# Kernel optimization log

Measured on AMD Instinct MI355X. Metric: run time of the kernel, lower is better.

The kernel has to match this reference:

```python
import jax, jax.numpy as jnp
import numpy as np

TAU = 0.05
BIG_POSITIVE = 1.0e10
COS_EPS = 1e-8  # torch F.cosine_similarity default eps


def setup_inputs() -> dict:
    key = jax.random.key(0)
    k1, k2 = jax.random.split(key)
    b, d = 4096, 1024
    return {
        "batch_feat1": jax.random.normal(k1, (b, d), dtype=jnp.float32),
        "batch_feat2": jax.random.normal(k2, (b, d), dtype=jnp.float32),
        "input_mask": jnp.zeros((b,), dtype=jnp.int32),
    }


def reference(batch_feat1, batch_feat2, input_mask):
    # concat the two views: (2b, d)
    feat = jnp.concatenate([batch_feat1, batch_feat2], axis=0)
    bs = feat.shape[0]
    half = bs // 2

    # cosine similarity = normalize (clamped norm, as in torch) then GEMM
    norm = jnp.maximum(jnp.linalg.norm(feat, axis=-1, keepdims=True), COS_EPS)
    n = feat / norm
    similarity = n @ n.T  # (2b, 2b)

    # mask out self-similarity on the diagonal
    eye = jnp.eye(bs, dtype=similarity.dtype)
    logits = similarity / TAU - eye * BIG_POSITIVE

    idx = jnp.arange(half)
    y_true = jnp.concatenate([idx + half, idx])  # positive pair indices

    # weighted cross entropy: weight[c] = 1 - input_mask[c] (per-class weight)
    weight = (1 - jnp.concatenate([input_mask, input_mask], axis=0)).astype(logits.dtype)
    logp = jax.nn.log_softmax(logits, axis=-1)
    per_example = -jnp.take_along_axis(logp, y_true[:, None], axis=1)[:, 0]
    w = weight[y_true]
    loss = jnp.sum(w * per_example) / jnp.sum(w)
    return (loss, logits, y_true)
```

## Files before the change

kernel.cpp:

```cpp
#include <hip/hip_runtime.h>
#include <math.h>

#define BS 8192
#define HALF 4096
#define DIM 1024
#define BIGP 1.0e10f
#define SQRT_TAU_INV 4.472135955f
#define BK 64
#define NT (DIM / BK)

typedef __attribute__((ext_vector_type(8))) short bf16x8;
typedef __attribute__((ext_vector_type(4))) float f32x4;

#define GLOAD_LDS16(g, l)                                              \
    __builtin_amdgcn_global_load_lds(                                  \
        (const __attribute__((address_space(1))) void*)(g),            \
        (__attribute__((address_space(3))) void*)(l), 16, 0, 0)

__device__ inline unsigned short f2bf(float f) {
    union { float f; unsigned int u; } c; c.f = f;
    unsigned int u = c.u;
    u += 0x7FFFu + ((u >> 16) & 1u);
    return (unsigned short)(u >> 16);
}

__global__ __launch_bounds__(256) void norm_kernel(const float* __restrict__ f1,
                                                   const float* __restrict__ f2,
                                                   unsigned short* __restrict__ nb) {
    const int row = blockIdx.x;
    const int t = threadIdx.x;
    const float* src = (row < HALF) ? (f1 + (size_t)row * DIM)
                                    : (f2 + (size_t)(row - HALF) * DIM);
    float4 v = reinterpret_cast<const float4*>(src)[t];
    float ss = v.x * v.x + v.y * v.y + v.z * v.z + v.w * v.w;
#pragma unroll
    for (int off = 32; off > 0; off >>= 1) ss += __shfl_down(ss, off, 64);
    __shared__ float red[4];
    if ((t & 63) == 0) red[t >> 6] = ss;
    __syncthreads();
    float tot = red[0] + red[1] + red[2] + red[3];
    float inv = SQRT_TAU_INV / fmaxf(sqrtf(tot), 1e-8f);
    ushort4 o;
    o.x = f2bf(v.x * inv);
    o.y = f2bf(v.y * inv);
    o.z = f2bf(v.z * inv);
    o.w = f2bf(v.w * inv);
    reinterpret_cast<ushort4*>(nb + (size_t)row * DIM)[t] = o;
}

__global__ __launch_bounds__(512, 2) void gemm_kernel(const unsigned short* __restrict__ nb,
                                                      float* __restrict__ logits,
                                                      float* __restrict__ psum,
                                                      float* __restrict__ targ) {
    __shared__ unsigned short As[2][256][BK];
    __shared__ unsigned short Bs[2][256][BK];

    const int t = threadIdx.x;
    const int lane = t & 63;
    const int wid = t >> 6;
    const int wr = wid >> 2;
    const int wcn = wid & 3;
    const int lo = lane & 15;
    const int hi = lane >> 4;

    const int id = blockIdx.x;
    int bx = (int)((sqrtf(8.0f * (float)id + 1.0f) - 1.0f) * 0.5f);
    while ((bx + 1) * (bx + 2) / 2 <= id) ++bx;
    while (bx * (bx + 1) / 2 > id) --bx;
    const int by = id - bx * (bx + 1) / 2;
    const bool diag = (bx == by);

    const int rowBase = by * 256;
    const int colBase = bx * 256;

    f32x4 acc[8][4];
#pragma unroll
    for (int m = 0; m < 8; ++m)
#pragma unroll
        for (int n = 0; n < 4; ++n) {
            acc[m][n][0] = 0.f; acc[m][n][1] = 0.f;
            acc[m][n][2] = 0.f; acc[m][n][3] = 0.f;
        }

    const int srow = lane >> 3;
    const int skoff = (((lane & 7) ^ srow) << 3);
    const int rswz = (lo & 7) << 4;

#define STAGE(kti, b) do {                                                       \
    const int kt_ = (kti) * BK;                                                  \
    _Pragma("unroll")                                                            \
    for (int i_ = 0; i_ < 4; ++i_) {                                             \
        const int chunk_ = wid * 4 + i_;                \
        const int r_ = chunk_ * 8 + srow;                                        \
        GLOAD_LDS16(nb + (size_t)(rowBase + r_) * DIM + kt_ + skoff,             \
                    (char*)&As[b][0][0] + chunk_ * 1024);                        \
        GLOAD_LDS16(nb + (size_t)(colBase + r_) * DIM + kt_ + skoff,             \
                    (char*)&Bs[b][0][0] + chunk_ * 1024);                        \
    } } while (0)

#define COMPUTE(cur) do {                                                        \
    const char* Ab = (const char*)&As[cur][0][0];                                \
    const char* Bb = (const char*)&Bs[cur][0][0];                                \
    bf16x8 bf[4][2];                                                             \
    _Pragma("unroll")                                                            \
    for (int n_ = 0; n_ < 4; ++n_)                                               \
        _Pragma("unroll")                                                        \
        for (int k2 = 0; k2 < 2; ++k2)                                           \
            bf[n_][k2] = *reinterpret_cast<const bf16x8*>(                       \
                Bb + (wcn * 64 + n_ * 16 + lo) * 128 + ((k2 * 64 + hi * 16) ^ rswz)); \
    _Pragma("unroll")                                                            \
    for (int q_ = 0; q_ < 4; ++q_) {                                             \
        bf16x8 af[2][2];                                                         \
        _Pragma("unroll")                                                        \
        for (int mm = 0; mm < 2; ++mm)                                           \
            _Pragma("unroll")                                                    \
            for (int k2 = 0; k2 < 2; ++k2)                                       \
                af[mm][k2] = *reinterpret_cast<const bf16x8*>(                   \
                    Ab + (wr * 128 + (q_ * 2 + mm) * 16 + lo) * 128 +            \
                         ((k2 * 64 + hi * 16) ^ rswz));                          \
        __builtin_amdgcn_s_setprio(1);                                           \
        _Pragma("unroll")                                                        \
        for (int mm = 0; mm < 2; ++mm)                                           \
            _Pragma("unroll")                                                    \
            for (int n_ = 0; n_ < 4; ++n_)                                       \
                _Pragma("unroll")                                                \
                for (int k2 = 0; k2 < 2; ++k2)                                   \
                    acc[q_ * 2 + mm][n_] = __builtin_amdgcn_mfma_f32_16x16x32_bf16( \
                        af[mm][k2], bf[n_][k2], acc[q_ * 2 + mm][n_], 0, 0, 0);  \
        __builtin_amdgcn_s_setprio(0);                                           \
    } } while (0)

    STAGE(0, 0);
    STAGE(1, 1);

    for (int kt = 0; kt < NT - 1; ++kt) {
        const int cur = kt & 1;
        asm volatile("s_waitcnt vmcnt(8)" ::: "memory");
        __builtin_amdgcn_s_barrier();
        asm volatile("" ::: "memory");
        COMPUTE(cur);
        asm volatile("" ::: "memory");
        __builtin_amdgcn_s_barrier();
        asm volatile("" ::: "memory");
        if (kt + 2 < NT) STAGE(kt + 2, cur);
    }
    asm volatile("s_waitcnt vmcnt(0)" ::: "memory");
    __builtin_amdgcn_s_barrier();
    asm volatile("" ::: "memory");
    COMPUTE((NT - 1) & 1);

    if (diag) {
#pragma unroll
        for (int m = 0; m < 8; ++m) {
            const int lr0 = wr * 128 + m * 16 + hi * 4;
#pragma unroll
            for (int n = 0; n < 4; ++n) {
                const int lc = wcn * 64 + n * 16 + lo;
#pragma unroll
                for (int r = 0; r < 4; ++r)
                    if (lr0 + r == lc) acc[m][n][r] -= BIGP;
            }
        }
    }

    float sums[32];
    float psn[4] = {0.f, 0.f, 0.f, 0.f};
#pragma unroll
    for (int p = 0; p < 32; ++p) sums[p] = 0.f;

#pragma unroll
    for (int m = 0; m < 8; ++m) {
        const int trow0 = rowBase + wr * 128 + m * 16 + hi * 4;
#pragma unroll
        for (int n = 0; n < 4; ++n) {
            const int col = colBase + wcn * 64 + n * 16 + lo;
#pragma unroll
            for (int r = 0; r < 4; ++r) {
                const int row = trow0 + r;
                const float v = acc[m][n][r];
                logits[(size_t)row * BS + col] = v;
                if (col == row + HALF) { targ[row] = v; targ[col] = v; }
                const float e = __expf(v - 20.0f);
                sums[m * 4 + r] += e;
                psn[n] += e;
            }
        }
    }

    if (!diag) {
#pragma unroll
        for (int m = 0; m < 8; ++m) {
            const int trow0 = rowBase + wr * 128 + m * 16 + hi * 4;
#pragma unroll
            for (int n = 0; n < 4; ++n) {
                const int col = colBase + wcn * 64 + n * 16 + lo;
                *reinterpret_cast<f32x4*>(&logits[(size_t)col * BS + trow0]) = acc[m][n];
            }
        }
    }

    float sel0 = 0.f, sel1 = 0.f;
#pragma unroll
    for (int p = 0; p < 16; ++p) {
        float sv = sums[p];
        sv += __shfl_xor(sv, 1, 64);
        sv += __shfl_xor(sv, 2, 64);
        sv += __shfl_xor(sv, 4, 64);
        sv += __shfl_xor(sv, 8, 64);
        sel0 = (lo == p) ? sv : sel0;
    }
#pragma unroll
    for (int p = 0; p < 16; ++p) {
        float sv = sums[16 + p];
        sv += __shfl_xor(sv, 1, 64);
        sv += __shfl_xor(sv, 2, 64);
        sv += __shfl_xor(sv, 4, 64);
        sv += __shfl_xor(sv, 8, 64);
        sel1 = (lo == p) ? sv : sel1;
    }
    const int base_r = rowBase + wr * 128 + (lo >> 2) * 16 + hi * 4 + (lo & 3);
    psum[(size_t)(4 * bx + wcn) * BS + base_r] = sel0;
    psum[(size_t)(4 * bx + wcn) * BS + base_r + 64] = sel1;

    if (!diag) {
#pragma unroll
        for (int n = 0; n < 4; ++n) {
            psn[n] += __shfl_xor(psn[n], 16, 64);
            psn[n] += __shfl_xor(psn[n], 32, 64);
        }
        const float cw = (hi == 0) ? psn[0] : (hi == 1) ? psn[1]
                       : (hi == 2) ? psn[2] : psn[3];
        psum[(size_t)(128 + 2 * by + wr) * BS + colBase + wcn * 64 + hi * 16 + lo] = cw;
    }
#undef STAGE
#undef COMPUTE
}

__global__ __launch_bounds__(256) void reduce_rows_kernel(const float* __restrict__ psum,
                                                          const float* __restrict__ targ,
                                                          const int* __restrict__ mask,
                                                          float* __restrict__ partials,
                                                          float* __restrict__ ytrue_out) {
    const int t = threadIdx.x;
    const int row = blockIdx.x * 256 + t;
    const int rb = row >> 8;

    float total = 0.f;
    for (int s = 4 * rb; s < 128; ++s) total += psum[(size_t)s * BS + row];
    for (int s = 0; s < 2 * rb; ++s) total += psum[(size_t)(128 + s) * BS + row];

    const float pe = -(targ[row] - 20.0f - logf(total));
    const float w = 1.0f - (float)mask[row & (HALF - 1)];
    ytrue_out[row] = (float)((row < HALF) ? row + HALF : row - HALF);

    float a = w * pe, b = w;
#pragma unroll
    for (int off = 32; off > 0; off >>= 1) {
        a += __shfl_down(a, off, 64);
        b += __shfl_down(b, off, 64);
    }
    __shared__ float ra[4], rb_[4];
    if ((t & 63) == 0) { ra[t >> 6] = a; rb_[t >> 6] = b; }
    __syncthreads();
    if (t == 0) {
        partials[blockIdx.x] = ra[0] + ra[1] + ra[2] + ra[3];
        partials[32 + blockIdx.x] = rb_[0] + rb_[1] + rb_[2] + rb_[3];
    }
}

__global__ void loss_kernel(const float* __restrict__ partials,
                            float* __restrict__ loss_out) {
    if (threadIdx.x == 0) {
        float A = 0.f, B = 0.f;
        for (int i = 0; i < 32; ++i) { A += partials[i]; B += partials[32 + i]; }
        loss_out[0] = A / B;
    }
}

extern "C" void kernel_launch(void* const* d_in, const int* in_sizes, int n_in,
                              void* d_out, int out_size, void* d_ws, size_t ws_size,
                              hipStream_t stream) {
    const float* f1 = (const float*)d_in[0];
    const float* f2 = (const float*)d_in[1];
    const int* mask = (const int*)d_in[2];
    float* out = (float*)d_out;

    unsigned short* nb = (unsigned short*)d_ws;
    float* psum = (float*)((char*)d_ws + (size_t)BS * DIM * 2);
    float* targ = psum + (size_t)192 * BS;
    float* partials = targ + BS;
    float* logits = out + 1;
    float* ytrue_out = out + 1 + (size_t)BS * BS;

    norm_kernel<<<BS, 256, 0, stream>>>(f1, f2, nb);

    const int ntri = 32 * 33 / 2;
    gemm_kernel<<<ntri, 512, 0, stream>>>(nb, logits, psum, targ);

    reduce_rows_kernel<<<BS / 256, 256, 0, stream>>>(psum, targ, mask, partials, ytrue_out);
    loss_kernel<<<1, 64, 0, stream>>>(partials, out);
}
```

Baseline: 196.0 us.

## Interleave half-tile global-to-LDS loads with per-quarter MFMA phases in GEMM

Restructures the GEMM main loop so the A and B tile loads are split into half-tiles and issued between the four MFMA quarter-phases. Each phase is bracketed by barriers, with finer vmcnt waits. The goal is to spread memory traffic across compute and keep the load and matrix pipes overlapped. The launch bound drops the min-2-blocks occupancy hint, which may change register allocation. The extra barriers per tile add synchronisation overhead and could cost more than the overlap gains.

```diff
diff --git a/kernel.cpp b/kernel.cpp
--- a/kernel.cpp
+++ b/kernel.cpp
@@ -16,6 +16,8 @@
     __builtin_amdgcn_global_load_lds(                                  \
         (const __attribute__((address_space(1))) void*)(g),            \
         (__attribute__((address_space(3))) void*)(l), 16, 0, 0)
+
+#define FENCE() asm volatile("" ::: "memory")
 
 __device__ inline unsigned short f2bf(float f) {
     union { float f; unsigned int u; } c; c.f = f;
@@ -48,10 +50,10 @@
     reinterpret_cast<ushort4*>(nb + (size_t)row * DIM)[t] = o;
 }
 
-__global__ __launch_bounds__(512, 2) void gemm_kernel(const unsigned short* __restrict__ nb,
-                                                      float* __restrict__ logits,
-                                                      float* __restrict__ psum,
-                                                      float* __restrict__ targ) {
+__global__ __launch_bounds__(512) void gemm_kernel(const unsigned short* __restrict__ nb,
+                                                   float* __restrict__ logits,
+                                                   float* __restrict__ psum,
+                                                   float* __restrict__ targ) {
     __shared__ unsigned short As[2][256][BK];
     __shared__ unsigned short Bs[2][256][BK];
 
@@ -86,68 +88,108 @@
     const int skoff = (((lane & 7) ^ srow) << 3);
     const int rswz = (lo & 7) << 4;
 
-#define STAGE(kti, b) do {                                                       \
-    const int kt_ = (kti) * BK;                                                  \
-    _Pragma("unroll")                                                            \
-    for (int i_ = 0; i_ < 4; ++i_) {                                             \
-        const int chunk_ = wid * 4 + i_;                \
-        const int r_ = chunk_ * 8 + srow;                                        \
-        GLOAD_LDS16(nb + (size_t)(rowBase + r_) * DIM + kt_ + skoff,             \
-                    (char*)&As[b][0][0] + chunk_ * 1024);                        \
-        GLOAD_LDS16(nb + (size_t)(colBase + r_) * DIM + kt_ + skoff,             \
-                    (char*)&Bs[b][0][0] + chunk_ * 1024);                        \
+#define STAGE_HALF(tile, baseRow, half, dstbase) do {                          \
+    const int kt_ = (tile) * BK;                                               \
+    _Pragma("unroll")                                                          \
+    for (int c_ = 0; c_ < 2; ++c_) {                                           \
+        const int r_ = (half) * 128 + c_ * 64 + wid * 8 + srow;                \
+        GLOAD_LDS16(nb + (size_t)((baseRow) + r_) * DIM + kt_ + skoff,         \
+                    (char*)(dstbase) + (size_t)(half) * 16384 + c_ * 8192 + wid * 1024); \
     } } while (0)
 
-#define COMPUTE(cur) do {                                                        \
-    const char* Ab = (const char*)&As[cur][0][0];                                \
-    const char* Bb = (const char*)&Bs[cur][0][0];                                \
-    bf16x8 bf[4][2];                                                             \
-    _Pragma("unroll")                                                            \
-    for (int n_ = 0; n_ < 4; ++n_)                                               \
-        _Pragma("unroll")                                                        \
-        for (int k2 = 0; k2 < 2; ++k2)                                           \
-            bf[n_][k2] = *reinterpret_cast<const bf16x8*>(                       \
-                Bb + (wcn * 64 + n_ * 16 + lo) * 128 + ((k2 * 64 + hi * 16) ^ rswz)); \
-    _Pragma("unroll")                                                            \
-    for (int q_ = 0; q_ < 4; ++q_) {                                             \
-        bf16x8 af[2][2];                                                         \
-        _Pragma("unroll")                                                        \
-        for (int mm = 0; mm < 2; ++mm)                                           \
-            _Pragma("unroll")                                                    \
-            for (int k2 = 0; k2 < 2; ++k2)                                       \
-                af[mm][k2] = *reinterpret_cast<const bf16x8*>(                   \
-                    Ab + (wr * 128 + (q_ * 2 + mm) * 16 + lo) * 128 +            \
-                         ((k2 * 64 + hi * 16) ^ rswz));                          \
-        __builtin_amdgcn_s_setprio(1);                                           \
-        _Pragma("unroll")                                                        \
-        for (int mm = 0; mm < 2; ++mm)                                           \
-            _Pragma("unroll")                                                    \
-            for (int n_ = 0; n_ < 4; ++n_)                                       \
-                _Pragma("unroll")                                                \
-                for (int k2 = 0; k2 < 2; ++k2)                                   \
-                    acc[q_ * 2 + mm][n_] = __builtin_amdgcn_mfma_f32_16x16x32_bf16( \
-                        af[mm][k2], bf[n_][k2], acc[q_ * 2 + mm][n_], 0, 0, 0);  \
-        __builtin_amdgcn_s_setprio(0);                                           \
-    } } while (0)
-
-    STAGE(0, 0);
-    STAGE(1, 1);
-
-    for (int kt = 0; kt < NT - 1; ++kt) {
-        const int cur = kt & 1;
-        asm volatile("s_waitcnt vmcnt(8)" ::: "memory");
-        __builtin_amdgcn_s_barrier();
-        asm volatile("" ::: "memory");
-        COMPUTE(cur);
-        asm volatile("" ::: "memory");
-        __builtin_amdgcn_s_barrier();
-        asm volatile("" ::: "memory");
-        if (kt + 2 < NT) STAGE(kt + 2, cur);
-    }
-    asm volatile("s_waitcnt vmcnt(0)" ::: "memory");
-    __builtin_amdgcn_s_barrier();
-    asm volatile("" ::: "memory");
-    COMPUTE((NT - 1) & 1);
+#define LOAD_BF(bf, Bb) do {                                                   \
+    _Pragma("unroll")                                                          \
+    for (int n_ = 0; n_ < 4; ++n_)                                             \
+        _Pragma("unroll")                                                      \
+        for (int k2 = 0; k2 < 2; ++k2)                                         \
+            bf[n_][k2] = *reinterpret_cast<const bf16x8*>(                     \
+                (const char*)(Bb) + (wcn * 64 + n_ * 16 + lo) * 128 +          \
+                ((k2 * 64 + hi * 16) ^ rswz));                                 \
+    } while (0)
+
+#define LOAD_AF(af, Ab, q) do {                                                \
+    _Pragma("unroll")                                                          \
+    for (int mm = 0; mm < 2; ++mm)                                             \
+        _Pragma("unroll")                                                      \
+        for (int k2 = 0; k2 < 2; ++k2)                                         \
+            af[mm][k2] = *reinterpret_cast<const bf16x8*>(                     \
+                (const char*)(Ab) + (wr * 128 + ((q) * 2 + mm) * 16 + lo) * 128 + \
+                ((k2 * 64 + hi * 16) ^ rswz));                                 \
+    } while (0)
+
+#define MFMA16(af, bf, q) do {                                                 \
+    __builtin_amdgcn_s_setprio(1);                                             \
+    _Pragma("unroll")                                                          \
+    for (int mm = 0; mm < 2; ++mm)                                             \
+        _Pragma("unroll")                                                      \
+        for (int n_ = 0; n_ < 4; ++n_)                                         \
+            _Pragma("unroll")                                                  \
+            for (int k2 = 0; k2 < 2; ++k2)                                     \
+                acc[(q) * 2 + mm][n_] = __builtin_amdgcn_mfma_f32_16x16x32_bf16( \
+                    af[mm][k2], bf[n_][k2], acc[(q) * 2 + mm][n_], 0, 0, 0);   \
+    __builtin_amdgcn_s_setprio(0);                                             \
+    } while (0)
+
+#define BARRIER() do { FENCE(); __builtin_amdgcn_s_barrier(); FENCE(); } while (0)
+
+    STAGE_HALF(0, rowBase, 0, &As[0][0][0]);
+    STAGE_HALF(0, rowBase, 1, &As[0][0][0]);
+    STAGE_HALF(0, colBase, 0, &Bs[0][0][0]);
+    STAGE_HALF(0, colBase, 1, &Bs[0][0][0]);
+    STAGE_HALF(1, colBase, 0, &Bs[1][0][0]);
+    STAGE_HALF(1, colBase, 1, &Bs[1][0][0]);
+    asm volatile("s_waitcnt vmcnt(4)" ::: "memory");
+    BARRIER();
+
+    for (int i = 0; i < NT / 2; ++i) {
+        const int a = 2 * i, b = 2 * i + 1;
+        const bool last = (i == NT / 2 - 1);
+
+        {
+            bf16x8 bf[4][2];
+#pragma unroll
+            for (int q = 0; q < 4; ++q) {
+                if (q == 0) LOAD_BF(bf, &Bs[0][0][0]);
+                bf16x8 af[2][2];
+                LOAD_AF(af, &As[0][0][0], q);
+                if (q == 0) STAGE_HALF(b, rowBase, 0, &As[1][0][0]);
+                else if (q == 1) STAGE_HALF(b, rowBase, 1, &As[1][0][0]);
+                else if (q == 2) { if (!last) STAGE_HALF(a + 2, colBase, 0, &Bs[0][0][0]); }
+                else {
+                    if (!last) {
+                        STAGE_HALF(a + 2, colBase, 1, &Bs[0][0][0]);
+                        asm volatile("s_waitcnt vmcnt(4)" ::: "memory");
+                    } else {
+                        asm volatile("s_waitcnt vmcnt(0)" ::: "memory");
+                    }
+                }
+                BARRIER();
+                MFMA16(af, bf, q);
+                BARRIER();
+            }
+        }
+        {
+            bf16x8 bf[4][2];
+#pragma unroll
+            for (int q = 0; q < 4; ++q) {
+                if (q == 0) LOAD_BF(bf, &Bs[1][0][0]);
+                bf16x8 af[2][2];
+                LOAD_AF(af, &As[1][0][0], q);
+                if (q == 0) { if (!last) STAGE_HALF(a + 2, rowBase, 0, &As[0][0][0]); }
+                else if (q == 1) { if (!last) STAGE_HALF(a + 2, rowBase, 1, &As[0][0][0]); }
+                else if (q == 2) { if (!last) STAGE_HALF(b + 2, colBase, 0, &Bs[1][0][0]); }
+                else {
+                    if (!last) {
+                        STAGE_HALF(b + 2, colBase, 1, &Bs[1][0][0]);
+                        asm volatile("s_waitcnt vmcnt(4)" ::: "memory");
+                    }
+                }
+                BARRIER();
+                MFMA16(af, bf, q);
+                BARRIER();
+            }
+        }
+    }
 
     if (diag) {
 #pragma unroll
@@ -232,8 +274,11 @@
                        : (hi == 2) ? psn[2] : psn[3];
         psum[(size_t)(128 + 2 * by + wr) * BS + colBase + wcn * 64 + hi * 16 + lo] = cw;
     }
-#undef STAGE
-#undef COMPUTE
+#undef STAGE_HALF
+#undef LOAD_BF
+#undef LOAD_AF
+#undef MFMA16
+#undef BARRIER
 }
 
 __global__ __launch_bounds__(256) void reduce_rows_kernel(const float* __restrict__ psum,
```

Result: faster. 190.7 us (-2.7%).
